# Performance work log

Measured on AMD Instinct MI355X. Metric: run time of the kernel, lower is better.

The kernel has to match this reference:

```python
import jax, jax.numpy as jnp
import numpy as np
from jax import lax

WINDOW = 512
HOP = 128
SR = 16000
ALPHA = 1e-06
F = WINDOW // 2 + 1  # 257 bins
GAIN = float(np.sqrt(8.0 / 3.0))

# frequency-domain constants (match PsychoacousticMasker properties)
_freqs = np.linspace(0.0, SR / 2.0, F)
_bark_np = 13.0 * np.arctan(0.00076 * _freqs) + 3.5 * np.arctan((_freqs / 7500.0) ** 2)
_valid_dom = (_freqs >= 20.0) & (_freqs <= 20000.0)
_ath_np = np.full(F, -np.inf)
_fk = _freqs[_valid_dom] * 0.001
_ath_np[_valid_dom] = 3.64 * _fk ** -0.8 - 6.5 * np.exp(-0.6 * (_fk - 3.3) ** 2) + 0.001 * _fk ** 4 - 12.0
BARK = jnp.asarray(_bark_np, jnp.float32)
ATH = jnp.asarray(_ath_np, jnp.float32)
DELTA_SHIFT = -6.025 - 0.275 * BARK
HANN = jnp.asarray(0.5 * (1.0 - np.cos(2.0 * np.pi * np.arange(WINDOW) / WINDOW)), jnp.float32)


def _stft(x):
    # center=False hann STFT -> [n_frames, F] complex
    n_frames = (x.shape[0] - WINDOW) // HOP + 1
    idx = jnp.arange(n_frames)[:, None] * HOP + jnp.arange(WINDOW)[None, :]
    return jnp.fft.rfft(x[idx] * HANN, axis=-1)


def _frame_threshold(p):
    # p: [F] SPL-normalized PSD (dB) for one frame -> global masking threshold [F]
    interior = (p[1:-1] > p[:-2]) & (p[1:-1] > p[2:])
    is_max = jnp.pad(interior, (1, 1), constant_values=False)
    pw = 10.0 ** (p / 10.0)
    m_all = 10.0 * jnp.log10(pw + jnp.roll(pw, 1) + jnp.roll(pw, -1))  # tonal masker level (bins j-1,j,j+1)
    valid = is_max & (m_all > ATH)
    order = jnp.argsort((~valid).astype(jnp.int32))  # stable: valid bins first, in frequency order
    vmask = valid[order]
    m_c = jnp.where(vmask, m_all[order], -200.0)     # compacted masker dB values
    n = valid.sum()

    def step(carry, i):
        i_prev, keep = carry
        active = i < n
        # NB: source indexes bark[] with masker *list positions* (i, i_prev); replicated faithfully
        close = (BARK[i] - BARK[i_prev]) < 0.5
        prev_smaller = m_c[i_prev] < m_c[i]
        del_idx = jnp.where(prev_smaller, i_prev, i)
        keep = jnp.where(active & close, keep.at[del_idx].set(False), keep)
        i_prev = jnp.where(active, jnp.where(close, jnp.where(prev_smaller, i_prev + 1, i_prev), i), i_prev)
        return (i_prev, keep), None

    (_, keep), _ = lax.scan(step, (jnp.int32(0), jnp.ones(F, dtype=bool)), jnp.arange(1, F, dtype=jnp.int32))
    keep = keep & vmask
    # individual thresholds, vectorized over maskers k and bins
    z_j = BARK[order]                                    # bark of each masker's bin
    dz = BARK[None, :] - z_j[:, None]                    # [K, F]
    slope = jnp.where(dz > 0, -27.0 + 0.37 * jnp.maximum(m_c - 40.0, 0.0)[:, None], 27.0)
    t = m_c[:, None] + DELTA_SHIFT[order][:, None] + slope * dz
    power = jnp.where(keep[:, None], 10.0 ** (t / 10.0), 0.0)
    return 10.0 * jnp.log10(power.sum(0) + 10.0 ** (ATH / 10.0))


def _threshold_and_psd_max(audio):
    s = _stft(audio)                                     # [T, F]
    psd = 20.0 * jnp.log10(jnp.abs(GAIN * s / WINDOW))
    psd = jnp.maximum(psd, -200.0)
    psd_max = psd.max()
    psd_n = 96.0 - psd_max + psd
    thr = jax.vmap(_frame_threshold)(psd_n)              # [T, F]
    return thr, psd_max


def setup_inputs() -> dict:
    key = jax.random.key(0)
    k1, k2 = jax.random.split(key)
    L = 160000  # 10 s @ 16 kHz; (L - 512) % 128 == 0 -> 1247 frames, pad is a no-op
    x_ref = 0.5 * jax.random.normal(k1, (L,), dtype=jnp.float32)
    x_adv = x_ref + 0.01 * jax.random.normal(k2, (L,), dtype=jnp.float32)
    return {"x_adv": x_adv, "x_ref": x_ref}


def reference(x_adv, x_ref):
    thr, psd_max = _threshold_and_psd_max(x_ref)
    thr = lax.stop_gradient(thr)
    psd_max = lax.stop_gradient(psd_max)
    delta = x_adv - x_ref
    sd = _stft(delta)                                    # [T, F]
    psd_d = (GAIN / WINDOW) ** 2 * (sd.real ** 2 + sd.imag ** 2)
    psd_d = (10.0 ** 9.6) / (10.0 ** (psd_max / 10.0)) * psd_d
    loss = jnp.mean(jax.nn.relu(psd_d - 10.0 ** (thr / 10.0)))
    return ALPHA * loss
```

## Files before the change

### kernel.cpp

```cpp
#include <hip/hip_runtime.h>
#include <math.h>


#define FBINS 257

#define TAB_BARK  0
#define TAB_ATHDB 257
#define TAB_ATHP  514
#define TAB_HANN  771
#define TAB_TWR   1283
#define TAB_TWI   1539
#define TAB_FLOATS 2048

__global__ __launch_bounds__(256) void k0_init(float* __restrict__ tab)
{
    const int tid = threadIdx.x;
    const double TWO_PI = 6.283185307179586476925286766559;
    if (blockIdx.x == 0) {
        for (int f = tid; f < FBINS; f += 256) {
            double freq = 31.25 * (double)f;
            double q    = freq / 7500.0;
            tab[TAB_BARK + f] = (float)(13.0 * atan(0.00076 * freq) + 3.5 * atan(q * q));
            if (f == 0) {
                tab[TAB_ATHDB] = -INFINITY;
                tab[TAB_ATHP]  = 0.0f;
            } else {
                double fk = freq * 0.001;
                double ad = 3.64 * pow(fk, -0.8)
                          - 6.5 * exp(-0.6 * (fk - 3.3) * (fk - 3.3))
                          + 0.001 * fk * fk * fk * fk - 12.0;
                float av = (float)ad;
                tab[TAB_ATHDB + f] = av;
                tab[TAB_ATHP  + f] = exp10f(av / 10.0f);
            }
        }
    } else if (blockIdx.x == 1) {
        for (int n = tid; n < 512; n += 256) {
            double cw = cos((TWO_PI * (double)n) / 512.0);
            tab[TAB_HANN + n] = (float)(0.5 * (1.0 - cw));
        }
    } else {
        for (int j = tid; j < 256; j += 256) {
            double s, c;
            sincos(-(TWO_PI / 512.0) * (double)j, &s, &c);
            tab[TAB_TWR + j] = (float)c;
            tab[TAB_TWI + j] = (float)s;
        }
    }
}

__global__ __launch_bounds__(256) void k1_stft(
    const float* __restrict__ xadv, const float* __restrict__ xref,
    const float* __restrict__ tab,
    float* __restrict__ psd_db, float* __restrict__ pd, float* __restrict__ fmaxs)
{
    __shared__ float2 tw2[256];
    __shared__ float2 bufA[256], bufB[256];
    __shared__ float2 zf[512];
    __shared__ float wmax[4];
    const int t = blockIdx.x, tid = threadIdx.x;

    tw2[tid] = make_float2(tab[TAB_TWR + tid], tab[TAB_TWI + tid]);

    const int base_idx = t * 128;
    const int n0 = (int)(__brev((unsigned)tid) >> 24);
    const int n1 = n0 + 256;
    float w0 = tab[TAB_HANN + n0], w1 = tab[TAB_HANN + n1];
    float r0 = xref[base_idx + n0], r1 = xref[base_idx + n1];
    float a0 = xadv[base_idx + n0], a1 = xadv[base_idx + n1];
    float2 E0 = make_float2(w0 * r0, w0 * (a0 - r0));
    float2 E1 = make_float2(w1 * r1, w1 * (a1 - r1));
    __syncthreads();

    #pragma unroll
    for (int s = 1; s <= 7; ++s) {
        const int half  = 1 << (s - 1);
        const int tstep = 512 >> s;
        float2 w = tw2[(tid & (half - 1)) * tstep];
        float vr = E1.x * w.x - E1.y * w.y;
        float vi = E1.x * w.y + E1.y * w.x;
        float ur = E0.x, ui = E0.y;
        E0 = make_float2(ur + vr, ui + vi);
        E1 = make_float2(ur - vr, ui - vi);
        if (s <= 6) {
            const int d = 1 << (s - 1);
            int b = (tid >> (s - 1)) & 1;
            float2 keep = b ? E1 : E0;
            float2 send = b ? E0 : E1;
            float2 recv;
            recv.x = __shfl_xor(send.x, d);
            recv.y = __shfl_xor(send.y, d);
            E0 = b ? recv : keep;
            E1 = b ? keep : recv;
        }
    }
    {
        int b = (tid >> 6) & 1;
        float2 keep = b ? E1 : E0;
        bufA[tid] = b ? E0 : E1;
        __syncthreads();
        float2 recv = bufA[tid ^ 64];
        E0 = b ? recv : keep;
        E1 = b ? keep : recv;
    }
    {
        float2 w = tw2[(tid & 127) * 2];
        float vr = E1.x * w.x - E1.y * w.y;
        float vi = E1.x * w.y + E1.y * w.x;
        float ur = E0.x, ui = E0.y;
        E0 = make_float2(ur + vr, ui + vi);
        E1 = make_float2(ur - vr, ui - vi);
    }
    {
        int b = (tid >> 7) & 1;
        float2 keep = b ? E1 : E0;
        bufB[tid] = b ? E0 : E1;
        __syncthreads();
        float2 recv = bufB[tid ^ 128];
        E0 = b ? recv : keep;
        E1 = b ? keep : recv;
    }
    {
        float2 w = tw2[tid];
        float vr = E1.x * w.x - E1.y * w.y;
        float vi = E1.x * w.y + E1.y * w.x;
        float ur = E0.x, ui = E0.y;
        E0 = make_float2(ur + vr, ui + vi);
        E1 = make_float2(ur - vr, ui - vi);
    }
    zf[tid]       = E0;
    zf[tid + 256] = E1;
    __syncthreads();

    const float S2 = 1.0172526041666667e-05f;
    float lmax = -1e30f;
    for (int k = tid; k <= 256; k += 256) {
        int nk = (512 - k) & 511;
        float2 zk = zf[k];
        float2 zn = zf[nk];
        float ar = 0.5f * (zk.x + zn.x), ai = 0.5f * (zk.y - zn.y);
        float br = 0.5f * (zk.y + zn.y), bi = 0.5f * (zn.x - zk.x);
        float prefp = S2 * (ar * ar + ai * ai);
        float pdb   = fmaxf(10.0f * log10f(prefp), -200.0f);
        psd_db[t * FBINS + k] = pdb;
        pd[t * FBINS + k]     = S2 * (br * br + bi * bi);
        lmax = fmaxf(lmax, pdb);
    }
    for (int off = 32; off > 0; off >>= 1) lmax = fmaxf(lmax, __shfl_down(lmax, off));
    if ((tid & 63) == 0) wmax[tid >> 6] = lmax;
    __syncthreads();
    if (tid == 0)
        fmaxs[t] = fmaxf(fmaxf(wmax[0], wmax[1]), fmaxf(wmax[2], wmax[3]));
}

__global__ __launch_bounds__(256) void k3_threshold(
    const float* __restrict__ tab,
    const float* __restrict__ psd_db, const float* __restrict__ pd,
    const float* __restrict__ fmaxs, int nf, float* __restrict__ floss)
{
    __shared__ float barkf[FBINS], athp_s[FBINS];
    __shared__ float p_s[FBINS], pw_s[FBINS];
    __shared__ float mc_s[128], shift_s[128], barkm_s[128], ups_s[128];
    __shared__ int   bin_s[128], keep_s[128];
    __shared__ float2 pmk[132];
    __shared__ int   wcnt[4];
    __shared__ float red[4];
    __shared__ float sm[4];

    const int t = blockIdx.x, tid = threadIdx.x;
    const int lane = tid & 63, wid = tid >> 6;

    const float pdb_a = psd_db[t * FBINS + tid];
    const float pdb_b = psd_db[t * FBINS + 256];

    for (int f = tid; f < FBINS; f += 256) {
        barkf[f]  = tab[TAB_BARK + f];
        athp_s[f] = tab[TAB_ATHP + f];
    }
    float v = -1e30f;
    for (int i = tid; i < nf; i += 256) v = fmaxf(v, fmaxs[i]);
    for (int off = 32; off > 0; off >>= 1) v = fmaxf(v, __shfl_down(v, off));
    if (lane == 0) sm[wid] = v;
    __syncthreads();
    const float pmax   = fmaxf(fmaxf(sm[0], sm[1]), fmaxf(sm[2], sm[3]));
    const float shift0 = 96.0f - pmax;

    {
        float pv = shift0 + pdb_a;
        p_s[tid]  = pv;
        pw_s[tid] = exp10f(pv / 10.0f);
        if (tid == 0) {
            float pv2 = shift0 + pdb_b;
            p_s[256]  = pv2;
            pw_s[256] = exp10f(pv2 / 10.0f);
        }
    }
    __syncthreads();

    float m = -1e30f;
    int   pred = 0;
    if (tid >= 1 && tid <= 255) {
        float pc = p_s[tid];
        if (pc > p_s[tid - 1] && pc > p_s[tid + 1]) {
            m = 10.0f * log10f((pw_s[tid] + pw_s[tid - 1]) + pw_s[tid + 1]);
            if (m > tab[TAB_ATHDB + tid]) pred = 1;
        }
    }
    unsigned long long bal = __ballot(pred);
    if (lane == 0) wcnt[wid] = __popcll(bal);
    __syncthreads();
    int base = 0;
    for (int w = 0; w < wid; ++w) base += wcnt[w];
    const int n_total = wcnt[0] + wcnt[1] + wcnt[2] + wcnt[3];
    if (pred) {
        int pos = base + __popcll(bal & ((1ull << lane) - 1));
        bin_s[pos] = tid; mc_s[pos] = m; keep_s[pos] = 1;
    }
    __syncthreads();

    if (tid <= n_total && tid < 130) {
        pmk[tid] = (tid < n_total) ? make_float2(barkf[tid], mc_s[tid])
                                   : make_float2(1.0e30f, -1.0e30f);
    }
    __syncthreads();

    if (tid == 0 && n_total > 1) {
        int   i_prev = 0;
        float bp = pmk[0].x, mp = pmk[0].y;
        float2 c = pmk[1];
        for (int i = 1; i < n_total; ++i) {
            float2 nx = pmk[i + 1];
            bool close        = (c.x - bp) < 0.5f;
            bool prev_smaller = mp < c.y;
            if (close) {
                keep_s[prev_smaller ? i_prev : i] = 0;
                if (prev_smaller) {
                    ++i_prev;
                    if (i_prev == i) { bp = c.x; mp = c.y; }
                    else { float2 p = pmk[i_prev]; bp = p.x; mp = p.y; }
                }
            } else {
                i_prev = i; bp = c.x; mp = c.y;
            }
            c = nx;
        }
    }
    __syncthreads();

    int pred2 = (tid < n_total) && keep_s[tid];
    unsigned long long bal2 = __ballot(pred2);
    if (lane == 0) wcnt[wid] = __popcll(bal2);
    __syncthreads();
    int base2 = 0;
    for (int w = 0; w < wid; ++w) base2 += wcnt[w];
    const int nk = wcnt[0] + wcnt[1] + wcnt[2] + wcnt[3];
    if (pred2) {
        int pos = base2 + __popcll(bal2 & ((1ull << lane) - 1));
        int   fb = bin_s[tid];
        float mc = mc_s[tid];
        shift_s[pos] = mc + (-6.025f - 0.275f * barkf[fb]);
        barkm_s[pos] = barkf[fb];
        ups_s[pos]   = -27.0f + 0.37f * fmaxf(mc - 40.0f, 0.0f);
    }
    __syncthreads();

    const float C = 3981071705.534973f / exp10f(pmax / 10.0f);
    float lsum = 0.0f;
    for (int f = tid; f < FBINS; f += 256) {
        float bf  = barkf[f];
        float acc = 0.0f;
        for (int k = 0; k < nk; ++k) {
            float dz    = bf - barkm_s[k];
            float slope = (dz > 0.0f) ? ups_s[k] : 27.0f;
            float tdb   = shift_s[k] + slope * dz;
            acc += exp10f(tdb / 10.0f);
        }
        float thrpow = acc + athp_s[f];
        float pds    = C * pd[t * FBINS + f];
        lsum += fmaxf(pds - thrpow, 0.0f);
    }
    for (int off = 32; off > 0; off >>= 1) lsum += __shfl_down(lsum, off);
    if ((tid & 63) == 0) red[tid >> 6] = lsum;
    __syncthreads();
    if (tid == 0) floss[t] = (red[0] + red[1]) + (red[2] + red[3]);
}

__global__ __launch_bounds__(256) void k4_final(
    const float* __restrict__ floss, int nf, float* __restrict__ out)
{
    __shared__ float red[4];
    float s = 0.0f;
    for (int i = threadIdx.x; i < nf; i += 256) s += floss[i];
    for (int off = 32; off > 0; off >>= 1) s += __shfl_down(s, off);
    if ((threadIdx.x & 63) == 0) red[threadIdx.x >> 6] = s;
    __syncthreads();
    if (threadIdx.x == 0) {
        float total = (red[0] + red[1]) + (red[2] + red[3]);
        out[0] = 1e-6f * (total / (float)(nf * FBINS));
    }
}

extern "C" void kernel_launch(void* const* d_in, const int* in_sizes, int n_in,
                              void* d_out, int out_size, void* d_ws, size_t ws_size,
                              hipStream_t stream)
{
    const float* x_adv = (const float*)d_in[0];
    const float* x_ref = (const float*)d_in[1];
    float*       out   = (float*)d_out;

    const int L  = in_sizes[0];
    const int nf = (L - 512) / 128 + 1;

    float* ws      = (float*)d_ws;
    float* tab     = ws;
    float* psd_db  = ws + TAB_FLOATS;
    float* pd      = psd_db + (size_t)nf * FBINS;
    float* fmaxs   = pd + (size_t)nf * FBINS;
    float* floss   = fmaxs + nf;

    k0_init     <<<3,  256, 0, stream>>>(tab);
    k1_stft     <<<nf, 256, 0, stream>>>(x_adv, x_ref, tab, psd_db, pd, fmaxs);
    k3_threshold<<<nf, 256, 0, stream>>>(tab, psd_db, pd, fmaxs, nf, floss);
    k4_final    <<<1,  256, 0, stream>>>(floss, nf, out);
}
```

Baseline: 85.04 us.

## Fuse STFT, threshold and final reduction into one cooperative kernel

Replaces the four-kernel pipeline with a single cooperative-launch kernel. Each block computes its frame's STFT, keeps the PSD and delta power in shared memory, and uses grid-wide syncs for the global max and the final loss sum. This removes launch overhead and the global-memory round trip of the per-frame PSD arrays. In exchange it adds two grid barriers, every block recomputes the Hann and twiddle tables, and the kernel relies on all 1247 blocks being co-resident (occupancy is checked against 256 CUs, with a fallback to the old path).

```diff
diff --git a/kernel.cpp b/kernel.cpp
--- a/kernel.cpp
+++ b/kernel.cpp
@@ -1,5 +1,8 @@
 #include <hip/hip_runtime.h>
+#include <hip/hip_cooperative_groups.h>
 #include <math.h>
+
+namespace cg = cooperative_groups;
 
 
 #define FBINS 257
@@ -11,6 +14,276 @@
 #define TAB_TWR   1283
 #define TAB_TWI   1539
 #define TAB_FLOATS 2048
+
+__global__ __launch_bounds__(256, 5) void kfused(
+    const float* __restrict__ xadv, const float* __restrict__ xref,
+    float* __restrict__ tab, float* __restrict__ fmaxs,
+    float* __restrict__ floss, int nf, float* __restrict__ out)
+{
+    __shared__ float  hannS[512];
+    __shared__ float2 tw2[256];
+    __shared__ float2 bufA[256], bufB[256];
+    __shared__ float2 zf[512];
+    __shared__ float  wmax[4];
+    __shared__ float  psdS[FBINS];
+    __shared__ float  pdS[FBINS];
+    __shared__ float  barkf[FBINS], athp_s[FBINS];
+    __shared__ float  p_s[FBINS], pw_s[FBINS];
+    __shared__ float  mc_s[128], shift_s[128], barkm_s[128], ups_s[128];
+    __shared__ int    bin_s[128], keep_s[128];
+    __shared__ float2 pmk[132];
+    __shared__ int    wcnt[4];
+    __shared__ float  red[4];
+    __shared__ float  sm[4];
+
+    const int t = blockIdx.x, tid = threadIdx.x;
+    const int lane = tid & 63, wid = tid >> 6;
+    const double TWO_PI = 6.283185307179586476925286766559;
+
+    for (int n = tid; n < 512; n += 256)
+        hannS[n] = (float)(0.5 * (1.0 - cos((TWO_PI * (double)n) / 512.0)));
+    {
+        double s, c;
+        sincos(-(TWO_PI / 512.0) * (double)tid, &s, &c);
+        tw2[tid] = make_float2((float)c, (float)s);
+    }
+    if (t == 0) {
+        for (int f = tid; f < FBINS; f += 256) {
+            double freq = 31.25 * (double)f;
+            double q    = freq / 7500.0;
+            tab[TAB_BARK + f] = (float)(13.0 * atan(0.00076 * freq) + 3.5 * atan(q * q));
+            if (f == 0) {
+                tab[TAB_ATHDB] = -INFINITY;
+                tab[TAB_ATHP]  = 0.0f;
+            } else {
+                double fk = freq * 0.001;
+                double ad = 3.64 * pow(fk, -0.8)
+                          - 6.5 * exp(-0.6 * (fk - 3.3) * (fk - 3.3))
+                          + 0.001 * fk * fk * fk * fk - 12.0;
+                float av = (float)ad;
+                tab[TAB_ATHDB + f] = av;
+                tab[TAB_ATHP  + f] = exp10f(av / 10.0f);
+            }
+        }
+    }
+    __syncthreads();
+
+    const int base_idx = t * 128;
+    const int n0 = (int)(__brev((unsigned)tid) >> 24);
+    const int n1 = n0 + 256;
+    float w0 = hannS[n0], w1 = hannS[n1];
+    float r0 = xref[base_idx + n0], r1 = xref[base_idx + n1];
+    float a0 = xadv[base_idx + n0], a1 = xadv[base_idx + n1];
+    float2 E0 = make_float2(w0 * r0, w0 * (a0 - r0));
+    float2 E1 = make_float2(w1 * r1, w1 * (a1 - r1));
+
+    #pragma unroll
+    for (int s = 1; s <= 7; ++s) {
+        const int half  = 1 << (s - 1);
+        const int tstep = 512 >> s;
+        float2 w = tw2[(tid & (half - 1)) * tstep];
+        float vr = E1.x * w.x - E1.y * w.y;
+        float vi = E1.x * w.y + E1.y * w.x;
+        float ur = E0.x, ui = E0.y;
+        E0 = make_float2(ur + vr, ui + vi);
+        E1 = make_float2(ur - vr, ui - vi);
+        if (s <= 6) {
+            const int d = 1 << (s - 1);
+            int b = (tid >> (s - 1)) & 1;
+            float2 keep = b ? E1 : E0;
+            float2 send = b ? E0 : E1;
+            float2 recv;
+            recv.x = __shfl_xor(send.x, d);
+            recv.y = __shfl_xor(send.y, d);
+            E0 = b ? recv : keep;
+            E1 = b ? keep : recv;
+        }
+    }
+    {
+        int b = (tid >> 6) & 1;
+        float2 keep = b ? E1 : E0;
+        bufA[tid] = b ? E0 : E1;
+        __syncthreads();
+        float2 recv = bufA[tid ^ 64];
+        E0 = b ? recv : keep;
+        E1 = b ? keep : recv;
+    }
+    {
+        float2 w = tw2[(tid & 127) * 2];
+        float vr = E1.x * w.x - E1.y * w.y;
+        float vi = E1.x * w.y + E1.y * w.x;
+        float ur = E0.x, ui = E0.y;
+        E0 = make_float2(ur + vr, ui + vi);
+        E1 = make_float2(ur - vr, ui - vi);
+    }
+    {
+        int b = (tid >> 7) & 1;
+        float2 keep = b ? E1 : E0;
+        bufB[tid] = b ? E0 : E1;
+        __syncthreads();
+        float2 recv = bufB[tid ^ 128];
+        E0 = b ? recv : keep;
+        E1 = b ? keep : recv;
+    }
+    {
+        float2 w = tw2[tid];
+        float vr = E1.x * w.x - E1.y * w.y;
+        float vi = E1.x * w.y + E1.y * w.x;
+        float ur = E0.x, ui = E0.y;
+        E0 = make_float2(ur + vr, ui + vi);
+        E1 = make_float2(ur - vr, ui - vi);
+    }
+    zf[tid]       = E0;
+    zf[tid + 256] = E1;
+    __syncthreads();
+
+    const float S2 = 1.0172526041666667e-05f;
+    float lmax = -1e30f;
+    for (int k = tid; k <= 256; k += 256) {
+        int nk = (512 - k) & 511;
+        float2 zk = zf[k];
+        float2 zn = zf[nk];
+        float ar = 0.5f * (zk.x + zn.x), ai = 0.5f * (zk.y - zn.y);
+        float br = 0.5f * (zk.y + zn.y), bi = 0.5f * (zn.x - zk.x);
+        float prefp = S2 * (ar * ar + ai * ai);
+        float pdb   = fmaxf(10.0f * log10f(prefp), -200.0f);
+        psdS[k] = pdb;
+        pdS[k]  = S2 * (br * br + bi * bi);
+        lmax = fmaxf(lmax, pdb);
+    }
+    for (int off = 32; off > 0; off >>= 1) lmax = fmaxf(lmax, __shfl_down(lmax, off));
+    if ((tid & 63) == 0) wmax[tid >> 6] = lmax;
+    __syncthreads();
+    if (tid == 0)
+        fmaxs[t] = fmaxf(fmaxf(wmax[0], wmax[1]), fmaxf(wmax[2], wmax[3]));
+
+    cg::this_grid().sync();
+
+    for (int f = tid; f < FBINS; f += 256) {
+        barkf[f]  = tab[TAB_BARK + f];
+        athp_s[f] = tab[TAB_ATHP + f];
+    }
+    float v = -1e30f;
+    for (int i = tid; i < nf; i += 256) v = fmaxf(v, fmaxs[i]);
+    for (int off = 32; off > 0; off >>= 1) v = fmaxf(v, __shfl_down(v, off));
+    if (lane == 0) sm[wid] = v;
+    __syncthreads();
+    const float pmax   = fmaxf(fmaxf(sm[0], sm[1]), fmaxf(sm[2], sm[3]));
+    const float shift0 = 96.0f - pmax;
+
+    {
+        float pv = shift0 + psdS[tid];
+        p_s[tid]  = pv;
+        pw_s[tid] = exp10f(pv / 10.0f);
+        if (tid == 0) {
+            float pv2 = shift0 + psdS[256];
+            p_s[256]  = pv2;
+            pw_s[256] = exp10f(pv2 / 10.0f);
+        }
+    }
+    __syncthreads();
+
+    float m = -1e30f;
+    int   pred = 0;
+    if (tid >= 1 && tid <= 255) {
+        float pc = p_s[tid];
+        if (pc > p_s[tid - 1] && pc > p_s[tid + 1]) {
+            m = 10.0f * log10f((pw_s[tid] + pw_s[tid - 1]) + pw_s[tid + 1]);
+            if (m > tab[TAB_ATHDB + tid]) pred = 1;
+        }
+    }
+    unsigned long long bal = __ballot(pred);
+    if (lane == 0) wcnt[wid] = __popcll(bal);
+    __syncthreads();
+    int base = 0;
+    for (int w = 0; w < wid; ++w) base += wcnt[w];
+    const int n_total = wcnt[0] + wcnt[1] + wcnt[2] + wcnt[3];
+    if (pred) {
+        int pos = base + __popcll(bal & ((1ull << lane) - 1));
+        bin_s[pos] = tid; mc_s[pos] = m; keep_s[pos] = 1;
+    }
+    __syncthreads();
+
+    if (tid <= n_total && tid < 130) {
+        pmk[tid] = (tid < n_total) ? make_float2(barkf[tid], mc_s[tid])
+                                   : make_float2(1.0e30f, -1.0e30f);
+    }
+    __syncthreads();
+
+    if (tid == 0 && n_total > 1) {
+        int   i_prev = 0;
+        float bp = pmk[0].x, mp = pmk[0].y;
+        float2 c = pmk[1];
+        for (int i = 1; i < n_total; ++i) {
+            float2 nx = pmk[i + 1];
+            bool close        = (c.x - bp) < 0.5f;
+            bool prev_smaller = mp < c.y;
+            if (close) {
+                keep_s[prev_smaller ? i_prev : i] = 0;
+                if (prev_smaller) {
+                    ++i_prev;
+                    if (i_prev == i) { bp = c.x; mp = c.y; }
+                    else { float2 p = pmk[i_prev]; bp = p.x; mp = p.y; }
+                }
+            } else {
+                i_prev = i; bp = c.x; mp = c.y;
+            }
+            c = nx;
+        }
+    }
+    __syncthreads();
+
+    int pred2 = (tid < n_total) && keep_s[tid];
+    unsigned long long bal2 = __ballot(pred2);
+    if (lane == 0) wcnt[wid] = __popcll(bal2);
+    __syncthreads();
+    int base2 = 0;
+    for (int w = 0; w < wid; ++w) base2 += wcnt[w];
+    const int nk2 = wcnt[0] + wcnt[1] + wcnt[2] + wcnt[3];
+    if (pred2) {
+        int pos = base2 + __popcll(bal2 & ((1ull << lane) - 1));
+        int   fb = bin_s[tid];
+        float mc = mc_s[tid];
+        shift_s[pos] = mc + (-6.025f - 0.275f * barkf[fb]);
+        barkm_s[pos] = barkf[fb];
+        ups_s[pos]   = -27.0f + 0.37f * fmaxf(mc - 40.0f, 0.0f);
+    }
+    __syncthreads();
+
+    const float C = 3981071705.534973f / exp10f(pmax / 10.0f);
+    float lsum = 0.0f;
+    for (int f = tid; f < FBINS; f += 256) {
+        float bf  = barkf[f];
+        float acc = 0.0f;
+        for (int k = 0; k < nk2; ++k) {
+            float dz    = bf - barkm_s[k];
+            float slope = (dz > 0.0f) ? ups_s[k] : 27.0f;
+            float tdb   = shift_s[k] + slope * dz;
+            acc += exp10f(tdb / 10.0f);
+        }
+        float thrpow = acc + athp_s[f];
+        float pds    = C * pdS[f];
+        lsum += fmaxf(pds - thrpow, 0.0f);
+    }
+    for (int off = 32; off > 0; off >>= 1) lsum += __shfl_down(lsum, off);
+    if ((tid & 63) == 0) red[tid >> 6] = lsum;
+    __syncthreads();
+    if (tid == 0) floss[t] = (red[0] + red[1]) + (red[2] + red[3]);
+
+    cg::this_grid().sync();
+
+    if (t == 0) {
+        float s2 = 0.0f;
+        for (int i = tid; i < nf; i += 256) s2 += floss[i];
+        for (int off = 32; off > 0; off >>= 1) s2 += __shfl_down(s2, off);
+        if ((tid & 63) == 0) red[tid >> 6] = s2;
+        __syncthreads();
+        if (tid == 0) {
+            float total = (red[0] + red[1]) + (red[2] + red[3]);
+            out[0] = 1e-6f * (total / (float)(nf * FBINS));
+        }
+    }
+}
 
 __global__ __launch_bounds__(256) void k0_init(float* __restrict__ tab)
 {
@@ -318,8 +591,29 @@
     float* fmaxs   = pd + (size_t)nf * FBINS;
     float* floss   = fmaxs + nf;
 
-    k0_init     <<<3,  256, 0, stream>>>(tab);
-    k1_stft     <<<nf, 256, 0, stream>>>(x_adv, x_ref, tab, psd_db, pd, fmaxs);
-    k3_threshold<<<nf, 256, 0, stream>>>(tab, psd_db, pd, fmaxs, nf, floss);
-    k4_final    <<<1,  256, 0, stream>>>(floss, nf, out);
+    static int maxB = -2;
+    if (maxB == -2) {
+        int mb = 0;
+        if (hipOccupancyMaxActiveBlocksPerMultiprocessor(&mb, kfused, 256, 0) == hipSuccess)
+            maxB = mb;
+        else
+            maxB = 0;
+    }
+
+    bool done = false;
+    if (maxB > 0 && (long long)maxB * 256 >= (long long)nf) {
+        int nf_i = nf;
+        void* kargs[] = { (void*)&x_adv, (void*)&x_ref, (void*)&tab,
+                          (void*)&fmaxs, (void*)&floss, (void*)&nf_i, (void*)&out };
+        hipError_t e = hipLaunchCooperativeKernel(kfused, dim3((unsigned)nf), dim3(256),
+                                                  kargs, 0u, stream);
+        done = (e == hipSuccess);
+    }
+
+    if (!done) {
+        k0_init     <<<3,  256, 0, stream>>>(tab);
+        k1_stft     <<<nf, 256, 0, stream>>>(x_adv, x_ref, tab, psd_db, pd, fmaxs);
+        k3_threshold<<<nf, 256, 0, stream>>>(tab, psd_db, pd, fmaxs, nf, floss);
+        k4_final    <<<1,  256, 0, stream>>>(floss, nf, out);
+    }
 }
```

New measurement: 84.99 us. No clear change (-0.1%).

## Compute each STFT frame's FFT within one wavefront using registers and shuffles

Applied to the files above, without the earlier changes.

The 512-point FFT moves from one frame per 256-thread block to one frame per 64-lane wavefront. Each lane holds 8 complex values in registers, so the first three stages run inside the lane and the later ones use cross-lane shuffles instead of shared-memory exchanges and block barriers. The twiddle table in shared memory gets an XOR swizzle to cut bank conflicts, and the per-frame max is reduced inside the wavefront. This removes the syncthreads and the LDS round trips and cuts the block count by four, at the cost of more registers per lane and more shuffle traffic.

```diff
diff --git a/kernel.cpp b/kernel.cpp
--- a/kernel.cpp
+++ b/kernel.cpp
@@ -51,106 +51,122 @@
 
 __global__ __launch_bounds__(256) void k1_stft(
     const float* __restrict__ xadv, const float* __restrict__ xref,
-    const float* __restrict__ tab,
+    const float* __restrict__ tab, int nf,
     float* __restrict__ psd_db, float* __restrict__ pd, float* __restrict__ fmaxs)
 {
-    __shared__ float2 tw2[256];
-    __shared__ float2 bufA[256], bufB[256];
-    __shared__ float2 zf[512];
-    __shared__ float wmax[4];
-    const int t = blockIdx.x, tid = threadIdx.x;
-
-    tw2[tid] = make_float2(tab[TAB_TWR + tid], tab[TAB_TWI + tid]);
-
-    const int base_idx = t * 128;
-    const int n0 = (int)(__brev((unsigned)tid) >> 24);
-    const int n1 = n0 + 256;
-    float w0 = tab[TAB_HANN + n0], w1 = tab[TAB_HANN + n1];
-    float r0 = xref[base_idx + n0], r1 = xref[base_idx + n1];
-    float a0 = xadv[base_idx + n0], a1 = xadv[base_idx + n1];
-    float2 E0 = make_float2(w0 * r0, w0 * (a0 - r0));
-    float2 E1 = make_float2(w1 * r1, w1 * (a1 - r1));
-    __syncthreads();
-
+    __shared__ float twr_s[256], twi_s[256];
+    const int tid = threadIdx.x, lane = tid & 63, wid = tid >> 6;
+
+    {
+        int a = tid;
+        int p = a ^ (a >> 5);
+        twr_s[p] = tab[TAB_TWR + a];
+        twi_s[p] = tab[TAB_TWI + a];
+    }
+    __syncthreads();
+
+    const int frame = blockIdx.x * 4 + wid;
+    if (frame >= nf) return;
+
+    const int base_idx = frame * 128;
+    const int nl = (int)(__brev((unsigned)lane) >> 26);
+    float2 E[8];
     #pragma unroll
-    for (int s = 1; s <= 7; ++s) {
-        const int half  = 1 << (s - 1);
-        const int tstep = 512 >> s;
-        float2 w = tw2[(tid & (half - 1)) * tstep];
-        float vr = E1.x * w.x - E1.y * w.y;
-        float vi = E1.x * w.y + E1.y * w.x;
-        float ur = E0.x, ui = E0.y;
-        E0 = make_float2(ur + vr, ui + vi);
-        E1 = make_float2(ur - vr, ui - vi);
-        if (s <= 6) {
-            const int d = 1 << (s - 1);
-            int b = (tid >> (s - 1)) & 1;
-            float2 keep = b ? E1 : E0;
-            float2 send = b ? E0 : E1;
-            float2 recv;
-            recv.x = __shfl_xor(send.x, d);
-            recv.y = __shfl_xor(send.y, d);
-            E0 = b ? recv : keep;
-            E1 = b ? keep : recv;
-        }
-    }
-    {
-        int b = (tid >> 6) & 1;
-        float2 keep = b ? E1 : E0;
-        bufA[tid] = b ? E0 : E1;
-        __syncthreads();
-        float2 recv = bufA[tid ^ 64];
-        E0 = b ? recv : keep;
-        E1 = b ? keep : recv;
-    }
-    {
-        float2 w = tw2[(tid & 127) * 2];
-        float vr = E1.x * w.x - E1.y * w.y;
-        float vi = E1.x * w.y + E1.y * w.x;
-        float ur = E0.x, ui = E0.y;
-        E0 = make_float2(ur + vr, ui + vi);
-        E1 = make_float2(ur - vr, ui - vi);
-    }
-    {
-        int b = (tid >> 7) & 1;
-        float2 keep = b ? E1 : E0;
-        bufB[tid] = b ? E0 : E1;
-        __syncthreads();
-        float2 recv = bufB[tid ^ 128];
-        E0 = b ? recv : keep;
-        E1 = b ? keep : recv;
-    }
-    {
-        float2 w = tw2[tid];
-        float vr = E1.x * w.x - E1.y * w.y;
-        float vi = E1.x * w.y + E1.y * w.x;
-        float ur = E0.x, ui = E0.y;
-        E0 = make_float2(ur + vr, ui + vi);
-        E1 = make_float2(ur - vr, ui - vi);
-    }
-    zf[tid]       = E0;
-    zf[tid + 256] = E1;
-    __syncthreads();
+    for (int j = 0; j < 8; ++j) {
+        int bj = (int)(__brev((unsigned)j) >> 29);
+        int n  = nl + (bj << 6);
+        float w = tab[TAB_HANN + n];
+        float r = xref[base_idx + n];
+        float a = xadv[base_idx + n];
+        E[j] = make_float2(w * r, w * (a - r));
+    }
+
+#define BFLY(U, V, WR, WI)                                   \
+    {                                                        \
+        float vr = (V).x * (WR) - (V).y * (WI);              \
+        float vi = (V).x * (WI) + (V).y * (WR);              \
+        float ur = (U).x, ui = (U).y;                        \
+        (U) = make_float2(ur + vr, ui + vi);                 \
+        (V) = make_float2(ur - vr, ui - vi);                 \
+    }
+
+    {
+        float wr = twr_s[0], wi = twi_s[0];
+        BFLY(E[0], E[1], wr, wi); BFLY(E[2], E[3], wr, wi);
+        BFLY(E[4], E[5], wr, wi); BFLY(E[6], E[7], wr, wi);
+    }
+    {
+        int p0 = 0 ^ (0 >> 5), p1 = 128 ^ (128 >> 5);
+        float wr0 = twr_s[p0], wi0 = twi_s[p0];
+        float wr1 = twr_s[p1], wi1 = twi_s[p1];
+        BFLY(E[0], E[2], wr0, wi0); BFLY(E[1], E[3], wr1, wi1);
+        BFLY(E[4], E[6], wr0, wi0); BFLY(E[5], E[7], wr1, wi1);
+    }
+    {
+        #pragma unroll
+        for (int pb = 0; pb < 4; ++pb) {
+            int a = pb * 64, p = a ^ (a >> 5);
+            float wr = twr_s[p], wi = twi_s[p];
+            BFLY(E[pb], E[pb + 4], wr, wi);
+        }
+    }
+    #pragma unroll
+    for (int s = 4; s <= 9; ++s) {
+        const int d    = 1 << (s - 4);
+        const int half = 1 << (s - 1);
+        const int tst  = 512 >> s;
+        const int b    = (lane >> (s - 4)) & 1;
+        #pragma unroll
+        for (int j = 0; j < 8; ++j) {
+            int a = ((8 * lane + j) & (half - 1)) * tst;
+            int p = a ^ (a >> 5);
+            float wr = twr_s[p], wi = twi_s[p];
+            float ox = __shfl_xor(E[j].x, d);
+            float oy = __shfl_xor(E[j].y, d);
+            float ux = b ? ox : E[j].x;
+            float uy = b ? oy : E[j].y;
+            float vx = b ? E[j].x : ox;
+            float vy = b ? E[j].y : oy;
+            float vr = vx * wr - vy * wi;
+            float vi = vx * wi + vy * wr;
+            E[j] = b ? make_float2(ux - vr, uy - vi)
+                     : make_float2(ux + vr, uy + vi);
+        }
+    }
+#undef BFLY
+
+    float2 Zn[8];
+    #pragma unroll
+    for (int j = 1; j < 8; ++j) {
+        Zn[j].x = __shfl_xor(E[8 - j].x, 63);
+        Zn[j].y = __shfl_xor(E[8 - j].y, 63);
+    }
+    {
+        int src = (64 - lane) & 63;
+        Zn[0].x = __shfl(E[0].x, src);
+        Zn[0].y = __shfl(E[0].y, src);
+    }
 
     const float S2 = 1.0172526041666667e-05f;
     float lmax = -1e30f;
-    for (int k = tid; k <= 256; k += 256) {
-        int nk = (512 - k) & 511;
-        float2 zk = zf[k];
-        float2 zn = zf[nk];
-        float ar = 0.5f * (zk.x + zn.x), ai = 0.5f * (zk.y - zn.y);
-        float br = 0.5f * (zk.y + zn.y), bi = 0.5f * (zn.x - zk.x);
-        float prefp = S2 * (ar * ar + ai * ai);
-        float pdb   = fmaxf(10.0f * log10f(prefp), -200.0f);
-        psd_db[t * FBINS + k] = pdb;
-        pd[t * FBINS + k]     = S2 * (br * br + bi * bi);
-        lmax = fmaxf(lmax, pdb);
+    if (lane <= 32) {
+        #pragma unroll
+        for (int j = 0; j < 8; ++j) {
+            int k = 8 * lane + j;
+            if (k <= 256) {
+                float2 zk = E[j], zn = Zn[j];
+                float ar = 0.5f * (zk.x + zn.x), ai = 0.5f * (zk.y - zn.y);
+                float br = 0.5f * (zk.y + zn.y), bi = 0.5f * (zn.x - zk.x);
+                float prefp = S2 * (ar * ar + ai * ai);
+                float pdb   = fmaxf(10.0f * log10f(prefp), -200.0f);
+                psd_db[frame * FBINS + k] = pdb;
+                pd[frame * FBINS + k]     = S2 * (br * br + bi * bi);
+                lmax = fmaxf(lmax, pdb);
+            }
+        }
     }
     for (int off = 32; off > 0; off >>= 1) lmax = fmaxf(lmax, __shfl_down(lmax, off));
-    if ((tid & 63) == 0) wmax[tid >> 6] = lmax;
-    __syncthreads();
-    if (tid == 0)
-        fmaxs[t] = fmaxf(fmaxf(wmax[0], wmax[1]), fmaxf(wmax[2], wmax[3]));
+    if (lane == 0) fmaxs[frame] = lmax;
 }
 
 __global__ __launch_bounds__(256) void k3_threshold(
@@ -318,8 +334,10 @@
     float* fmaxs   = pd + (size_t)nf * FBINS;
     float* floss   = fmaxs + nf;
 
-    k0_init     <<<3,  256, 0, stream>>>(tab);
-    k1_stft     <<<nf, 256, 0, stream>>>(x_adv, x_ref, tab, psd_db, pd, fmaxs);
-    k3_threshold<<<nf, 256, 0, stream>>>(tab, psd_db, pd, fmaxs, nf, floss);
-    k4_final    <<<1,  256, 0, stream>>>(floss, nf, out);
-}
+    const int k1_blocks = (nf + 3) / 4;
+
+    k0_init     <<<3,         256, 0, stream>>>(tab);
+    k1_stft     <<<k1_blocks, 256, 0, stream>>>(x_adv, x_ref, tab, nf, psd_db, pd, fmaxs);
+    k3_threshold<<<nf,        256, 0, stream>>>(tab, psd_db, pd, fmaxs, nf, floss);
+    k4_final    <<<1,         256, 0, stream>>>(floss, nf, out);
+}
```

Result: slower. 88.68 us (+4.3%).
